# Kernel tuning notes

Measured on AMD Instinct MI355X. Metric: run time of the kernel, lower is better.

The kernel has to match this reference:

```python
import jax, jax.numpy as jnp
import numpy as np

H = 3584        # hidden_size
NH = 16         # num_attention_heads
HD = 256        # head_dim
NKV = 8         # num_key_value_heads
GROUPS = NH // NKV
B, S = 2, 2048
SOFTCAP = 50.0
SCALE = 256.0 ** -0.5   # query_pre_attn_scalar ** -0.5
ROPE_BASE = 10000.0
NEG = -1e9


def _rotate_half(x):
    x1, x2 = jnp.split(x, 2, axis=-1)
    return jnp.concatenate([-x2, x1], axis=-1)


def _apply_rope(x, cos, sin):
    # x: [b, h, s, d]; cos/sin: [s, d]
    return x * cos[None, None] + _rotate_half(x) * sin[None, None]


def setup_inputs() -> dict:
    key = jax.random.key(0)
    k1, k2, k3, k4, k5 = jax.random.split(key, 5)
    hidden_states = jax.random.normal(k1, (B, S, H), dtype=jnp.float32)
    # additive causal mask [1, 1, S, S]
    causal = jnp.tril(jnp.ones((S, S), dtype=bool))
    attention_mask = jnp.where(causal, 0.0, NEG).astype(jnp.float32)[None, None]
    Wq = jax.random.normal(k2, (H, NH * HD), dtype=jnp.float32) * 0.02
    Wk = jax.random.normal(k3, (H, NKV * HD), dtype=jnp.float32) * 0.02
    Wv = jax.random.normal(k4, (H, NKV * HD), dtype=jnp.float32) * 0.02
    Wo = jax.random.normal(k5, (NH * HD, H), dtype=jnp.float32) * 0.02
    return {"hidden_states": hidden_states, "attention_mask": attention_mask,
            "Wq": Wq, "Wk": Wk, "Wv": Wv, "Wo": Wo}


def reference(hidden_states, attention_mask, Wq, Wk, Wv, Wo):
    b, s, _ = hidden_states.shape
    q = (hidden_states @ Wq).reshape(b, s, NH, HD).transpose(0, 2, 1, 3)   # [b,nh,s,d]
    k = (hidden_states @ Wk).reshape(b, s, NKV, HD).transpose(0, 2, 1, 3)  # [b,nkv,s,d]
    v = (hidden_states @ Wv).reshape(b, s, NKV, HD).transpose(0, 2, 1, 3)

    # RoPE (HF-style: freqs duplicated, rotate_half)
    pos = jnp.arange(s, dtype=jnp.float32)
    inv_freq = 1.0 / (ROPE_BASE ** (jnp.arange(0, HD, 2, dtype=jnp.float32) / HD))
    freqs = pos[:, None] * inv_freq[None, :]          # [s, d/2]
    emb = jnp.concatenate([freqs, freqs], axis=-1)    # [s, d]
    cos, sin = jnp.cos(emb), jnp.sin(emb)
    q = _apply_rope(q, cos, sin)
    k = _apply_rope(k, cos, sin)

    # repeat_kv for GQA
    k = jnp.repeat(k, GROUPS, axis=1)  # [b,nh,s,d]
    v = jnp.repeat(v, GROUPS, axis=1)

    scores = jnp.einsum('bhsd,bhtd->bhst', q, k) * SCALE
    # tanh logit softcapping
    scores = jnp.tanh(scores / SOFTCAP) * SOFTCAP
    scores = scores + attention_mask
    probs = jax.nn.softmax(scores.astype(jnp.float32), axis=-1).astype(q.dtype)
    out = jnp.einsum('bhst,bhtd->bhsd', probs, v)
    out = out.transpose(0, 2, 1, 3).reshape(b, s, NH * HD)
    return out @ Wo
```

## Files before the change

### kernel.cpp

```cpp
#include <hip/hip_runtime.h>
#include <cstdint>
#include <cstddef>

typedef __bf16 bf16x8 __attribute__((ext_vector_type(8)));
typedef unsigned short u16x8 __attribute__((ext_vector_type(8)));
typedef float  f32x4  __attribute__((ext_vector_type(4)));
typedef unsigned short u16;

#define GLDS16(GP, LP) __builtin_amdgcn_global_load_lds( \
    (const __attribute__((address_space(1))) void*)(GP), \
    (__attribute__((address_space(3))) void*)(LP), 16, 0, 0)

__device__ __forceinline__ float b2f(u16 u) {
  unsigned int x = ((unsigned int)u) << 16;
  return __builtin_bit_cast(float, x);
}
__device__ __forceinline__ u16 f2b(float f) {
  unsigned int u = __builtin_bit_cast(unsigned int, f);
  unsigned int r = (u + 0x7fffu + ((u >> 16) & 1u)) >> 16;
  return (u16)r;
}

constexpr int Bc  = 2;
constexpr int Sc  = 2048;
constexpr int Hc  = 3584;
constexpr int NHc = 16;
constexpr int HDc = 256;
constexpr int NKV = 8;
constexpr int QD  = NHc * HDc;
constexpr int QS  = 8192;
constexpr float SCALE   = 0.0625f;
constexpr float CAP     = 50.0f;
constexpr float INV_CAP = 1.0f / 50.0f;

__device__ __forceinline__ float softcap(float raw) {
  float y = raw * (SCALE * INV_CAP);
  float a = __builtin_fabsf(y);
  float e = __expf(-2.0f * a);
  float t = (1.0f - e) * __builtin_amdgcn_rcpf(1.0f + e);
  return copysignf(t, y) * CAP;
}

__global__ void rope_table_k(float* __restrict__ cosT, float* __restrict__ sinT) {
  int idx = blockIdx.x * 256 + threadIdx.x;
  int s = idx >> 7, i = idx & 127;
  float inv = expf((float)i * -0.0719557841560639f);
  float ang = (float)s * inv;
  cosT[idx] = cosf(ang);
  sinT[idx] = sinf(ang);
}

__global__ void cvt_f32_bf16(const float4* __restrict__ in, ushort4* __restrict__ out, int n4) {
  int i = blockIdx.x * 256 + threadIdx.x;
  int st = gridDim.x * 256;
  for (; i < n4; i += st) {
    float4 v = in[i];
    ushort4 u;
    u.x = f2b(v.x); u.y = f2b(v.y); u.z = f2b(v.z); u.w = f2b(v.w);
    out[i] = u;
  }
}

__global__ void transpose_cvt(const float* __restrict__ in, u16* __restrict__ out, int R, int C) {
  __shared__ float t[32][33];
  int c0 = blockIdx.x * 32, r0 = blockIdx.y * 32;
  int tx = threadIdx.x, ty = threadIdx.y;
#pragma unroll
  for (int i = 0; i < 4; i++)
    t[ty + i * 8][tx] = in[(size_t)(r0 + ty + i * 8) * C + c0 + tx];
  __syncthreads();
#pragma unroll
  for (int i = 0; i < 4; i++)
    out[(size_t)(c0 + ty + i * 8) * R + r0 + tx] = f2b(t[tx][ty + i * 8]);
}

__global__ void transpose_v(const u16* __restrict__ QKV, u16* __restrict__ Vt) {
  __shared__ u16 t[32][33];
  int b = blockIdx.z >> 3, kvh = blockIdx.z & 7;
  int s0 = blockIdx.x * 32, d0 = blockIdx.y * 32;
  int tx = threadIdx.x, ty = threadIdx.y;
#pragma unroll
  for (int i = 0; i < 4; i++)
    t[ty + i * 8][tx] = QKV[(size_t)(b * Sc + s0 + ty + i * 8) * QS + 6144 + kvh * HDc + d0 + tx];
  __syncthreads();
#pragma unroll
  for (int i = 0; i < 4; i++)
    Vt[(size_t)((b * NKV + kvh) * HDc + d0 + ty + i * 8) * Sc + s0 + tx] = t[tx][ty + i * 8];
}

template <int NH>
__global__ void rope_apply(u16* __restrict__ X, const float* __restrict__ cosT,
                           const float* __restrict__ sinT) {
  constexpr int LS = (NH == 16) ? 4 : 3;
  int idx = blockIdx.x * 256 + threadIdx.x;
  const int i4 = (idx & 31) << 2;
  const int h = (idx >> 5) & (NH - 1);
  const int row = idx >> (5 + LS);
  const int s = row & (Sc - 1);
  u16* p = X + (size_t)row * QS + h * 256 + i4;
  ushort4 lo = *(const ushort4*)p;
  ushort4 hi = *(const ushort4*)(p + 128);
  float4 c = *(const float4*)(cosT + s * 128 + i4);
  float4 sn = *(const float4*)(sinT + s * 128 + i4);
  ushort4 nlo, nhi;
  { float xl = b2f(lo.x), xh = b2f(hi.x);
    nlo.x = f2b(xl * c.x - xh * sn.x); nhi.x = f2b(xh * c.x + xl * sn.x); }
  { float xl = b2f(lo.y), xh = b2f(hi.y);
    nlo.y = f2b(xl * c.y - xh * sn.y); nhi.y = f2b(xh * c.y + xl * sn.y); }
  { float xl = b2f(lo.z), xh = b2f(hi.z);
    nlo.z = f2b(xl * c.z - xh * sn.z); nhi.z = f2b(xh * c.z + xl * sn.z); }
  { float xl = b2f(lo.w), xh = b2f(hi.w);
    nlo.w = f2b(xl * c.w - xh * sn.w); nhi.w = f2b(xh * c.w + xl * sn.w); }
  *(ushort4*)p = nlo;
  *(ushort4*)(p + 128) = nhi;
}

template <typename OT>
__global__ __launch_bounds__(512, 1) void gemm256(const u16* __restrict__ A,
                                                  const u16* __restrict__ Bt,
                                                  OT* __restrict__ C,
                                                  int M, int N, int K, int GM) {
  __shared__ alignas(16) u16 As[2][256 * 64];
  __shared__ alignas(16) u16 Bs[2][256 * 64];
  const int nwg = gridDim.x;
  const int cpx = nwg >> 3;
  const int wgid = (blockIdx.x & 7) * cpx + (blockIdx.x >> 3);
  const int GN = nwg / GM;
  const int width = 8 * GN;
  const int grp = wgid / width;
  const int rem = wgid - grp * width;
  const int m0 = (grp * 8 + (rem & 7)) * 256;
  const int n0 = (rem >> 3) * 256;
  const int tid = threadIdx.x;
  const int lane = tid & 63;
  const int w = tid >> 6;
  const int wm = w >> 2, wn = w & 3;
  const int lg = lane >> 4, lr = lane & 15;
  const int nkt = K >> 6;

  auto STAGE = [&](int buf, int kt) {
    const int k0 = kt * 64;
#pragma unroll
    for (int i = 0; i < 4; i++) {
      int c = i * 512 + tid;
      int row = c >> 3, slot = c & 7;
      GLDS16(A + (size_t)(m0 + row) * K + k0 + (slot ^ (row & 7)) * 8,
             (char*)As[buf] + c * 16);
    }
#pragma unroll
    for (int i = 0; i < 4; i++) {
      int c = i * 512 + tid;
      int row = c >> 3, slot = c & 7;
      GLDS16(Bt + (size_t)(n0 + row) * K + k0 + (slot ^ (row & 7)) * 8,
             (char*)Bs[buf] + c * 16);
    }
  };

  f32x4 acc[8][4] = {};

  STAGE(0, 0);
  STAGE(1, 1);
  asm volatile("s_waitcnt vmcnt(8)" ::: "memory");
  __builtin_amdgcn_sched_barrier(0);
  __builtin_amdgcn_s_barrier();

  for (int kt = 0; kt < nkt; ++kt) {
    const int buf = kt & 1;
    bf16x8 bfr[4][2], af[4][2], af2[4][2];
#pragma unroll
    for (int j = 0; j < 4; j++)
#pragma unroll
      for (int ks = 0; ks < 2; ks++) {
        int row = wn * 64 + j * 16 + lr;
        bfr[j][ks] = *(const bf16x8*)&Bs[buf][row * 64 + ((ks * 4 + lg) ^ (row & 7)) * 8];
      }
#pragma unroll
    for (int i = 0; i < 4; i++)
#pragma unroll
      for (int ks = 0; ks < 2; ks++) {
        int row = wm * 128 + i * 16 + lr;
        af[i][ks] = *(const bf16x8*)&As[buf][row * 64 + ((ks * 4 + lg) ^ (row & 7)) * 8];
      }
#pragma unroll
    for (int i = 0; i < 4; i++)
#pragma unroll
      for (int ks = 0; ks < 2; ks++) {
        int row = wm * 128 + 64 + i * 16 + lr;
        af2[i][ks] = *(const bf16x8*)&As[buf][row * 64 + ((ks * 4 + lg) ^ (row & 7)) * 8];
      }
    __builtin_amdgcn_s_setprio(1);
#pragma unroll
    for (int i = 0; i < 4; i++)
#pragma unroll
      for (int j = 0; j < 4; j++)
#pragma unroll
        for (int ks = 0; ks < 2; ks++)
          acc[i][j] = __builtin_amdgcn_mfma_f32_16x16x32_bf16(
              af[i][ks], bfr[j][ks], acc[i][j], 0, 0, 0);
    __builtin_amdgcn_s_setprio(0);
    asm volatile("s_waitcnt vmcnt(0) lgkmcnt(0)" ::: "memory");
    __builtin_amdgcn_sched_barrier(0);
    __builtin_amdgcn_s_barrier();
    if (kt + 2 < nkt) STAGE(buf, kt + 2);
    __builtin_amdgcn_s_setprio(1);
#pragma unroll
    for (int i = 0; i < 4; i++)
#pragma unroll
      for (int j = 0; j < 4; j++)
#pragma unroll
        for (int ks = 0; ks < 2; ks++)
          acc[4 + i][j] = __builtin_amdgcn_mfma_f32_16x16x32_bf16(
              af2[i][ks], bfr[j][ks], acc[4 + i][j], 0, 0, 0);
    __builtin_amdgcn_s_setprio(0);
  }

#pragma unroll
  for (int i = 0; i < 8; i++) {
    const int row = m0 + wm * 128 + i * 16 + lg * 4;
#pragma unroll
    for (int j = 0; j < 4; j++) {
      const int col = n0 + wn * 64 + j * 16 + lr;
#pragma unroll
      for (int r = 0; r < 4; r++) {
        if constexpr (sizeof(OT) == 2)
          C[(size_t)(row + r) * N + col] = f2b(acc[i][j][r]);
        else
          C[(size_t)(row + r) * N + col] = acc[i][j][r];
      }
    }
  }
}

__global__ __launch_bounds__(512) void attn_fwd(const u16* __restrict__ QKV,
                                                const u16* __restrict__ Vt,
                                                const float* __restrict__ cosT,
                                                const float* __restrict__ sinT,
                                                u16* __restrict__ AO) {
  constexpr int KVB = 64;
  __shared__ alignas(16) u16 Ks[KVB * 256];
  __shared__ alignas(16) u16 Vs[256 * KVB];
  __shared__ alignas(16) u16 Ps[8][16][64];
  const int bx = blockIdx.x, h = blockIdx.y, b = blockIdx.z;
  const int qt = b ? (15 - bx) : bx;
  const int q0 = qt * 128;
  const int kvh = h >> 1;
  const int tid = threadIdx.x, w = tid >> 6, lane = tid & 63;
  const int lg = lane >> 4, lr = lane & 15;
  const int myrow = q0 + w * 16 + lr;

  u16x8 qr[8];
  {
    const u16* qp = QKV + (size_t)(b * Sc + myrow) * QS + h * HDc + lg * 8;
#pragma unroll
    for (int kk = 0; kk < 8; kk++) qr[kk] = *(const u16x8*)(qp + kk * 32);
    const float* ct = cosT + myrow * 128 + lg * 8;
    const float* st = sinT + myrow * 128 + lg * 8;
#pragma unroll
    for (int kk = 0; kk < 4; kk++)
#pragma unroll
      for (int q4 = 0; q4 < 2; q4++) {
        float4 c = *(const float4*)(ct + kk * 32 + q4 * 4);
        float4 s = *(const float4*)(st + kk * 32 + q4 * 4);
#pragma unroll
        for (int e = 0; e < 4; e++) {
          int ei = q4 * 4 + e;
          float cc = (&c.x)[e], ss = (&s.x)[e];
          float lo = b2f(qr[kk][ei]), hi = b2f(qr[kk + 4][ei]);
          qr[kk][ei]     = f2b(lo * cc - hi * ss);
          qr[kk + 4][ei] = f2b(hi * cc + lo * ss);
        }
      }
  }
  bf16x8 qf[8];
#pragma unroll
  for (int kk = 0; kk < 8; kk++) qf[kk] = __builtin_bit_cast(bf16x8, qr[kk]);

  f32x4 o[16] = {};
  float m_r[4], l_r[4];
#pragma unroll
  for (int r = 0; r < 4; r++) { m_r[r] = -1e30f; l_r[r] = 0.0f; }
  const int my_qrow = q0 + w * 16 + lg * 4;
  const int wave_min_row = q0 + w * 16;
  const int wave_max_row = q0 + w * 16 + 15;

  const u16* kbase = QKV + (size_t)(b * Sc) * QS + 4096 + kvh * HDc;
  const u16* vbase = Vt + (size_t)((b * NKV + kvh) * HDc) * Sc;

  auto STAGE = [&](int t0) {
#pragma unroll
    for (int i = 0; i < 4; i++) {
      int c = i * 512 + tid;
      int row = c >> 5, slot = c & 31;
      GLDS16(kbase + (size_t)(t0 + row) * QS + (slot ^ (row & 7)) * 8, (char*)Ks + c * 16);
    }
#pragma unroll
    for (int i = 0; i < 4; i++) {
      int c = i * 512 + tid;
      int d = c >> 3, slot = c & 7;
      GLDS16(vbase + (size_t)d * Sc + t0 + (slot ^ (d & 7)) * 8, (char*)Vs + c * 16);
    }
  };

  const int nt = 2 * qt + 2;
  for (int ti = 0; ti < nt; ++ti) {
    const int t0 = ti * 64;
    STAGE(t0);
    asm volatile("s_waitcnt vmcnt(0)" ::: "memory");
    __builtin_amdgcn_sched_barrier(0);
    __builtin_amdgcn_s_barrier();

    if (t0 <= wave_max_row) {
      f32x4 sc[4];
#pragma unroll
      for (int j = 0; j < 4; j++) {
        f32x4 a = {0.f, 0.f, 0.f, 0.f};
        const int row = j * 16 + lr;
#pragma unroll
        for (int kk = 0; kk < 8; kk++) {
          int s0 = (kk * 4 + lg) ^ (lr & 7);
          bf16x8 kf = *(const bf16x8*)&Ks[row * 256 + s0 * 8];
          a = __builtin_amdgcn_mfma_f32_16x16x32_bf16(qf[kk], kf, a, 0, 0, 0);
        }
        sc[j] = a;
      }

      float tmax[4] = {-1e30f, -1e30f, -1e30f, -1e30f};
      if (t0 + 63 > wave_min_row) {
#pragma unroll
        for (int j = 0; j < 4; j++)
#pragma unroll
          for (int r = 0; r < 4; r++) {
            float x = softcap(sc[j][r]);
            if (t0 + j * 16 + lr > my_qrow + r) x = -1e9f;
            sc[j][r] = x;
            tmax[r] = fmaxf(tmax[r], x);
          }
      } else {
#pragma unroll
        for (int j = 0; j < 4; j++)
#pragma unroll
          for (int r = 0; r < 4; r++) {
            float x = softcap(sc[j][r]);
            sc[j][r] = x;
            tmax[r] = fmaxf(tmax[r], x);
          }
      }
#pragma unroll
      for (int xm = 1; xm < 16; xm <<= 1)
#pragma unroll
        for (int r = 0; r < 4; r++) tmax[r] = fmaxf(tmax[r], __shfl_xor(tmax[r], xm, 64));

      bool need = false;
#pragma unroll
      for (int r = 0; r < 4; r++) need |= (tmax[r] > m_r[r] + 8.0f);
      if (__any(need)) {
        float scal[4];
#pragma unroll
        for (int r = 0; r < 4; r++) {
          float mn = fmaxf(m_r[r], tmax[r]);
          scal[r] = __expf(m_r[r] - mn);
          m_r[r] = mn;
          l_r[r] *= scal[r];
        }
#pragma unroll
        for (int df = 0; df < 16; df++)
#pragma unroll
          for (int r = 0; r < 4; r++) o[df][r] *= scal[r];
      }

      float psum[4] = {0.f, 0.f, 0.f, 0.f};
#pragma unroll
      for (int j = 0; j < 4; j++)
#pragma unroll
        for (int r = 0; r < 4; r++) {
          float p = __expf(sc[j][r] - m_r[r]);
          psum[r] += p;
          int q = lg * 4 + r;
          Ps[w][q][(j * 16 + lr) ^ ((q & 7) << 3)] = f2b(p);
        }
#pragma unroll
      for (int xm = 1; xm < 16; xm <<= 1)
#pragma unroll
        for (int r = 0; r < 4; r++) psum[r] += __shfl_xor(psum[r], xm, 64);
#pragma unroll
      for (int r = 0; r < 4; r++) l_r[r] += psum[r];

      bf16x8 pf0 = *(const bf16x8*)&Ps[w][lr][(lg ^ (lr & 7)) * 8];
      bf16x8 pf1 = *(const bf16x8*)&Ps[w][lr][((lg ^ 4) ^ (lr & 7)) * 8];
#pragma unroll
      for (int df = 0; df < 16; df++) {
        const int d = df * 16 + lr;
        int s0 = lg ^ (d & 7);
        int s1 = (4 + lg) ^ (d & 7);
        bf16x8 vf0 = *(const bf16x8*)&Vs[d * KVB + s0 * 8];
        o[df] = __builtin_amdgcn_mfma_f32_16x16x32_bf16(pf0, vf0, o[df], 0, 0, 0);
        bf16x8 vf1 = *(const bf16x8*)&Vs[d * KVB + s1 * 8];
        o[df] = __builtin_amdgcn_mfma_f32_16x16x32_bf16(pf1, vf1, o[df], 0, 0, 0);
      }
    }

    __builtin_amdgcn_s_barrier();
  }

  float inv_l[4];
#pragma unroll
  for (int r = 0; r < 4; r++) inv_l[r] = 1.0f / l_r[r];
  u16* op = AO + (size_t)(b * Sc + my_qrow) * QD + h * HDc + lr;
#pragma unroll
  for (int df = 0; df < 16; df++)
#pragma unroll
    for (int r = 0; r < 4; r++)
      op[(size_t)r * QD + df * 16] = f2b(o[df][r] * inv_l[r]);
}

extern "C" void kernel_launch(void* const* d_in, const int* in_sizes, int n_in,
                              void* d_out, int out_size, void* d_ws, size_t ws_size,
                              hipStream_t stream) {
  (void)in_sizes; (void)n_in; (void)out_size; (void)ws_size;
  const float* hs = (const float*)d_in[0];
  const float* Wq = (const float*)d_in[2];
  const float* Wk = (const float*)d_in[3];
  const float* Wv = (const float*)d_in[4];
  const float* Wo = (const float*)d_in[5];
  float* out = (float*)d_out;
  char* ws = (char*)d_ws;

  float* cosT = (float*)(ws + 0);
  float* sinT = (float*)(ws + 1048576);
  u16* hsb    = (u16*)(ws + 2097152);
  u16* Wqkvt  = (u16*)(ws + 31457280);
  u16* Wot    = (u16*)(ws + 90177536);
  u16* QKVb   = (u16*)(ws + 119537664);
  u16* Vtr    = hsb;
  u16* AO     = Wqkvt;

  dim3 tb32x8(32, 8);

  rope_table_k<<<1024, 256, 0, stream>>>(cosT, sinT);
  cvt_f32_bf16<<<2048, 256, 0, stream>>>((const float4*)hs, (ushort4*)hsb, (Bc * Sc * Hc) / 4);
  transpose_cvt<<<dim3(QD / 32, Hc / 32), tb32x8, 0, stream>>>(Wq, Wqkvt, Hc, QD);
  transpose_cvt<<<dim3(2048 / 32, Hc / 32), tb32x8, 0, stream>>>(Wk, Wqkvt + (size_t)4096 * Hc, Hc, 2048);
  transpose_cvt<<<dim3(2048 / 32, Hc / 32), tb32x8, 0, stream>>>(Wv, Wqkvt + (size_t)6144 * Hc, Hc, 2048);
  transpose_cvt<<<dim3(Hc / 32, QD / 32), tb32x8, 0, stream>>>(Wo, Wot, QD, Hc);

  gemm256<u16><<<dim3(16 * 32), 512, 0, stream>>>(hsb, Wqkvt, QKVb, Bc * Sc, QS, Hc, 16);

  rope_apply<8><<<4096, 256, 0, stream>>>(QKVb + 4096, cosT, sinT);
  transpose_v<<<dim3(Sc / 32, HDc / 32, Bc * NKV), tb32x8, 0, stream>>>(QKVb, Vtr);

  attn_fwd<<<dim3(16, NHc, Bc), 512, 0, stream>>>(QKVb, Vtr, cosT, sinT, AO);

  gemm256<float><<<dim3(16 * 14), 512, 0, stream>>>(AO, Wot, out, Bc * Sc, Hc, QD, 16);
}
```

Before: 623.3 us.

## Double-buffer K/V tiles in attention and simplify softcap tanh

```diff
diff --git a/kernel.cpp b/kernel.cpp
--- a/kernel.cpp
+++ b/kernel.cpp
@@ -34,11 +34,8 @@
 constexpr float INV_CAP = 1.0f / 50.0f;
 
 __device__ __forceinline__ float softcap(float raw) {
-  float y = raw * (SCALE * INV_CAP);
-  float a = __builtin_fabsf(y);
-  float e = __expf(-2.0f * a);
-  float t = (1.0f - e) * __builtin_amdgcn_rcpf(1.0f + e);
-  return copysignf(t, y) * CAP;
+  float e = __expf(raw * (2.0f * SCALE * INV_CAP));
+  return CAP - (2.0f * CAP) * __builtin_amdgcn_rcpf(1.0f + e);
 }
 
 __global__ void rope_table_k(float* __restrict__ cosT, float* __restrict__ sinT) {
@@ -237,8 +234,8 @@
                                                 const float* __restrict__ sinT,
                                                 u16* __restrict__ AO) {
   constexpr int KVB = 64;
-  __shared__ alignas(16) u16 Ks[KVB * 256];
-  __shared__ alignas(16) u16 Vs[256 * KVB];
+  __shared__ alignas(16) u16 Ks[2][KVB * 256];
+  __shared__ alignas(16) u16 Vs[2][256 * KVB];
   __shared__ alignas(16) u16 Ps[8][16][64];
   const int bx = blockIdx.x, h = blockIdx.y, b = blockIdx.z;
   const int qt = b ? (15 - bx) : bx;
@@ -286,30 +283,41 @@
   const u16* kbase = QKV + (size_t)(b * Sc) * QS + 4096 + kvh * HDc;
   const u16* vbase = Vt + (size_t)((b * NKV + kvh) * HDc) * Sc;
 
-  auto STAGE = [&](int t0) {
+  auto STAGE = [&](int buf, int t0) {
 #pragma unroll
     for (int i = 0; i < 4; i++) {
       int c = i * 512 + tid;
       int row = c >> 5, slot = c & 31;
-      GLDS16(kbase + (size_t)(t0 + row) * QS + (slot ^ (row & 7)) * 8, (char*)Ks + c * 16);
+      GLDS16(kbase + (size_t)(t0 + row) * QS + (slot ^ (row & 7)) * 8,
+             (char*)Ks[buf] + c * 16);
     }
 #pragma unroll
     for (int i = 0; i < 4; i++) {
       int c = i * 512 + tid;
       int d = c >> 3, slot = c & 7;
-      GLDS16(vbase + (size_t)d * Sc + t0 + (slot ^ (d & 7)) * 8, (char*)Vs + c * 16);
+      GLDS16(vbase + (size_t)d * Sc + t0 + (slot ^ (d & 7)) * 8,
+             (char*)Vs[buf] + c * 16);
     }
   };
 
   const int nt = 2 * qt + 2;
+  int cur = 0;
+  STAGE(0, 0);
   for (int ti = 0; ti < nt; ++ti) {
     const int t0 = ti * 64;
-    STAGE(t0);
-    asm volatile("s_waitcnt vmcnt(0)" ::: "memory");
+    if (ti + 1 < nt) {
+      STAGE(cur ^ 1, t0 + 64);
+      asm volatile("s_waitcnt vmcnt(8)" ::: "memory");
+    } else {
+      asm volatile("s_waitcnt vmcnt(0)" ::: "memory");
+    }
     __builtin_amdgcn_sched_barrier(0);
     __builtin_amdgcn_s_barrier();
 
     if (t0 <= wave_max_row) {
+      const u16* KsT = Ks[cur];
+      const u16* VsT = Vs[cur];
+
       f32x4 sc[4];
 #pragma unroll
       for (int j = 0; j < 4; j++) {
@@ -318,7 +326,7 @@
 #pragma unroll
         for (int kk = 0; kk < 8; kk++) {
           int s0 = (kk * 4 + lg) ^ (lr & 7);
-          bf16x8 kf = *(const bf16x8*)&Ks[row * 256 + s0 * 8];
+          bf16x8 kf = *(const bf16x8*)&KsT[row * 256 + s0 * 8];
           a = __builtin_amdgcn_mfma_f32_16x16x32_bf16(qf[kk], kf, a, 0, 0, 0);
         }
         sc[j] = a;
@@ -392,14 +400,15 @@
         const int d = df * 16 + lr;
         int s0 = lg ^ (d & 7);
         int s1 = (4 + lg) ^ (d & 7);
-        bf16x8 vf0 = *(const bf16x8*)&Vs[d * KVB + s0 * 8];
+        bf16x8 vf0 = *(const bf16x8*)&VsT[d * KVB + s0 * 8];
         o[df] = __builtin_amdgcn_mfma_f32_16x16x32_bf16(pf0, vf0, o[df], 0, 0, 0);
-        bf16x8 vf1 = *(const bf16x8*)&Vs[d * KVB + s1 * 8];
+        bf16x8 vf1 = *(const bf16x8*)&VsT[d * KVB + s1 * 8];
         o[df] = __builtin_amdgcn_mfma_f32_16x16x32_bf16(pf1, vf1, o[df], 0, 0, 0);
       }
     }
 
     __builtin_amdgcn_s_barrier();
+    cur ^= 1;
   }
 
   float inv_l[4];
```

New measurement: 596.2 us (median of 2 runs). 1.05x faster.
